# Performance work log

Measured on AMD Instinct MI355X. Metric: run time of the kernel, lower is better.

Reference implementation:

```python
import jax, jax.numpy as jnp
import numpy as np

DIM = 1024
NUM_HEADS = 16
HEAD_DIM = DIM // NUM_HEADS
TOKENS_PER_FRAME = 1560


def setup_inputs() -> dict:
    key = jax.random.key(0)
    ks = jax.random.split(key, 10)
    B, T = 2, 16
    N = T * TOKENS_PER_FRAME
    s = 1.0 / np.sqrt(DIM)
    return {
        "x": jax.random.normal(ks[0], (B, N, DIM), dtype=jnp.float32),
        "c": jax.random.normal(ks[1], (B, T, DIM), dtype=jnp.float32),
        "Wq": jax.random.normal(ks[2], (DIM, DIM), dtype=jnp.float32) * s,
        "bq": jnp.zeros((DIM,), dtype=jnp.float32),
        "Wk": jax.random.normal(ks[3], (DIM, DIM), dtype=jnp.float32) * s,
        "bk": jnp.zeros((DIM,), dtype=jnp.float32),
        "Wv": jax.random.normal(ks[4], (DIM, DIM), dtype=jnp.float32) * s,
        "bv": jnp.zeros((DIM,), dtype=jnp.float32),
        "Wo": jax.random.normal(ks[5], (DIM, DIM), dtype=jnp.float32) * s,
        "bo": jnp.zeros((DIM,), dtype=jnp.float32),
    }


def reference(x, c, Wq, bq, Wk, bk, Wv, bv, Wo, bo):
    B, N, dim = x.shape
    T = c.shape[1]
    tpf = N // T
    H, hd = NUM_HEADS, HEAD_DIM
    scale = hd ** (-0.5)

    q = x @ Wq.T + bq            # [B, N, dim]
    k = c @ Wk.T + bk            # [B, T, dim]
    v = c @ Wv.T + bv            # [B, T, dim]

    qh = q.reshape(B, T, tpf, H, hd)
    kh = k.reshape(B, T, 1, H, hd)
    vh = v.reshape(B, T, 1, H, hd)

    # per-frame cross-attention with kv_len=1: scores [B,T,tpf,H,1]
    scores = (qh * kh).sum(-1, keepdims=True) * scale
    attn = jax.nn.softmax(scores, axis=-1)   # softmax over length-1 kv axis == 1.0
    out = attn * vh                          # broadcast v: [B,T,tpf,H,hd]

    out = out.reshape(B, N, dim)
    return out @ Wo.T + bo
```

## Files before the change

### kernel.cpp

```cpp
#include <hip/hip_runtime.h>
#include <hip/hip_bf16.h>


#define DIM    1024
#define K4     (DIM / 4)
#define MROWS  32
#define TPF    1560
#define CHUNK  13
#define SPLITS 120

typedef float fvec4 __attribute__((ext_vector_type(4)));

__global__ __launch_bounds__(256) void gemm_thin(const float* __restrict__ A,
                                                 const float* __restrict__ W,
                                                 const float* __restrict__ bias,
                                                 float* __restrict__ C) {
    const int wave = threadIdx.x >> 6;
    const int lane = threadIdx.x & 63;
    const int j0   = blockIdx.x * 2;
    const int r0   = wave * 8;

    const fvec4* __restrict__ A4 = (const fvec4*)A;
    const fvec4* __restrict__ W0 = (const fvec4*)(W + (size_t)j0 * DIM);
    const fvec4* __restrict__ W1 = (const fvec4*)(W + (size_t)(j0 + 1) * DIM);

    fvec4 wa[4], wb[4];
#pragma unroll
    for (int t = 0; t < 4; ++t) {
        wa[t] = W0[t * 64 + lane];
        wb[t] = W1[t * 64 + lane];
    }

    float accA[8], accB[8];
#pragma unroll
    for (int r = 0; r < 8; ++r) { accA[r] = 0.f; accB[r] = 0.f; }

#pragma unroll
    for (int r = 0; r < 8; ++r) {
        const fvec4* __restrict__ Ar = A4 + (size_t)(r0 + r) * K4;
#pragma unroll
        for (int t = 0; t < 4; ++t) {
            fvec4 a = Ar[t * 64 + lane];
            accA[r] += a.x * wa[t].x + a.y * wa[t].y + a.z * wa[t].z + a.w * wa[t].w;
            accB[r] += a.x * wb[t].x + a.y * wb[t].y + a.z * wb[t].z + a.w * wb[t].w;
        }
    }

#pragma unroll
    for (int r = 0; r < 8; ++r) {
        float va = accA[r], vb = accB[r];
#pragma unroll
        for (int off = 32; off > 0; off >>= 1) {
            va += __shfl_down(va, off, 64);
            vb += __shfl_down(vb, off, 64);
        }
        accA[r] = va; accB[r] = vb;
    }

    if (lane == 0) {
        const float b0 = bias[j0], b1 = bias[j0 + 1];
#pragma unroll
        for (int r = 0; r < 8; ++r) {
            C[(size_t)(r0 + r) * DIM + j0]     = accA[r] + b0;
            C[(size_t)(r0 + r) * DIM + j0 + 1] = accB[r] + b1;
        }
    }
}

__global__ __launch_bounds__(256) void bcast(const float* __restrict__ y,
                                             float* __restrict__ out) {
    const int bt = blockIdx.x / SPLITS;
    const int ch = blockIdx.x % SPLITS;

    const fvec4 val = ((const fvec4*)(y + (size_t)bt * DIM))[threadIdx.x];

    fvec4* o = (fvec4*)out + ((size_t)bt * TPF + (size_t)ch * CHUNK) * K4;
#pragma unroll
    for (int i = 0; i < CHUNK; ++i) {
        o[(size_t)i * K4 + threadIdx.x] = val;
    }
}

extern "C" void kernel_launch(void* const* d_in, const int* in_sizes, int n_in,
                              void* d_out, int out_size, void* d_ws, size_t ws_size,
                              hipStream_t stream) {
    const float* c  = (const float*)d_in[1];
    const float* Wv = (const float*)d_in[6];
    const float* bv = (const float*)d_in[7];
    const float* Wo = (const float*)d_in[8];
    const float* bo = (const float*)d_in[9];
    float* out = (float*)d_out;

    float* v = (float*)d_ws;
    float* y = (float*)d_ws + MROWS * DIM;

    gemm_thin<<<DIM / 2, 256, 0, stream>>>(c, Wv, bv, v);
    gemm_thin<<<DIM / 2, 256, 0, stream>>>(v, Wo, bo, y);
    bcast<<<MROWS * SPLITS, 256, 0, stream>>>(y, out);
}
```

Before: 329.8 us.

## Fuse output projection into broadcast kernel with nontemporal stores

Replaces the separate Wo GEMM and broadcast kernels with one kernel. Each block computes a 64-column slice of the projected per-frame vector and writes it across a chunk of frame rows using nontemporal stores. This removes a launch and the intermediate buffer, and aims to stream the large output write past the caches. In exchange, the Wo projection is recomputed redundantly for each row chunk, and each block writes narrower 256-byte row segments.

```diff
diff --git a/kernel.cpp b/kernel.cpp
--- a/kernel.cpp
+++ b/kernel.cpp
@@ -1,13 +1,13 @@
 #include <hip/hip_runtime.h>
-#include <hip/hip_bf16.h>
 
 
-#define DIM    1024
-#define K4     (DIM / 4)
-#define MROWS  32
-#define TPF    1560
-#define CHUNK  13
-#define SPLITS 120
+#define DIM     1024
+#define K4      (DIM / 4)
+#define MROWS   32
+#define TPF     1560
+#define JSLICES 16
+#define RCH     4
+#define RPB     (TPF / RCH)
 
 typedef float fvec4 __attribute__((ext_vector_type(4)));
 
@@ -67,17 +67,65 @@
     }
 }
 
-__global__ __launch_bounds__(256) void bcast(const float* __restrict__ y,
-                                             float* __restrict__ out) {
-    const int bt = blockIdx.x / SPLITS;
-    const int ch = blockIdx.x % SPLITS;
+__global__ __launch_bounds__(256) void gemm_bcast(const float* __restrict__ V,
+                                                  const float* __restrict__ Wo,
+                                                  const float* __restrict__ bo,
+                                                  float* __restrict__ out) {
+    const int jc = blockIdx.x % JSLICES;
+    const int rc = (blockIdx.x / JSLICES) % RCH;
+    const int bt = blockIdx.x / (JSLICES * RCH);
 
-    const fvec4 val = ((const fvec4*)(y + (size_t)bt * DIM))[threadIdx.x];
+    const int wave = threadIdx.x >> 6;
+    const int lane = threadIdx.x & 63;
+    const int jbase = jc * 64 + wave * 16;
 
-    fvec4* o = (fvec4*)out + ((size_t)bt * TPF + (size_t)ch * CHUNK) * K4;
+    const fvec4* __restrict__ V4 = (const fvec4*)(V + (size_t)bt * DIM);
+
+    fvec4 va[4];
 #pragma unroll
-    for (int i = 0; i < CHUNK; ++i) {
-        o[(size_t)i * K4 + threadIdx.x] = val;
+    for (int t = 0; t < 4; ++t) va[t] = V4[t * 64 + lane];
+
+    __shared__ float ys[64];
+
+    float acc[16];
+#pragma unroll
+    for (int cc = 0; cc < 16; ++cc) {
+        const fvec4* __restrict__ Wr = (const fvec4*)(Wo + (size_t)(jbase + cc) * DIM);
+        float s = 0.f;
+#pragma unroll
+        for (int t = 0; t < 4; ++t) {
+            fvec4 w = Wr[t * 64 + lane];
+            s += va[t].x * w.x + va[t].y * w.y + va[t].z * w.z + va[t].w * w.w;
+        }
+        acc[cc] = s;
+    }
+
+#pragma unroll
+    for (int cc = 0; cc < 16; ++cc) {
+        float s = acc[cc];
+#pragma unroll
+        for (int off = 32; off > 0; off >>= 1) s += __shfl_down(s, off, 64);
+        if (lane == 0) ys[wave * 16 + cc] = s + bo[jbase + cc];
+    }
+    __syncthreads();
+
+    const int fcol = threadIdx.x & 15;
+    const int rof  = threadIdx.x >> 4;
+    fvec4 val;
+    val.x = ys[fcol * 4 + 0];
+    val.y = ys[fcol * 4 + 1];
+    val.z = ys[fcol * 4 + 2];
+    val.w = ys[fcol * 4 + 3];
+
+    fvec4* o = (fvec4*)out
+             + ((size_t)bt * TPF + (size_t)rc * RPB) * K4
+             + (size_t)jc * 16 + fcol;
+#pragma unroll
+    for (int i = 0; i < 24; ++i) {
+        __builtin_nontemporal_store(val, o + (size_t)(rof + 16 * i) * K4);
+    }
+    if (rof < 6) {
+        __builtin_nontemporal_store(val, o + (size_t)(rof + 16 * 24) * K4);
     }
 }
 
@@ -92,9 +140,7 @@
     float* out = (float*)d_out;
 
     float* v = (float*)d_ws;
-    float* y = (float*)d_ws + MROWS * DIM;
 
     gemm_thin<<<DIM / 2, 256, 0, stream>>>(c, Wv, bv, v);
-    gemm_thin<<<DIM / 2, 256, 0, stream>>>(v, Wo, bo, y);
-    bcast<<<MROWS * SPLITS, 256, 0, stream>>>(y, out);
+    gemm_bcast<<<MROWS * RCH * JSLICES, 256, 0, stream>>>(v, Wo, bo, out);
 }
```

New measurement: 365.8 us. 10.9% more time.
